# Kernel tuning notes

Hardware: AMD Instinct MI355X
Metric: run time of the kernel (lower is better)

The kernel has to match this reference:

```python
import jax, jax.numpy as jnp
import numpy as np

EMBED_DIM = 512
NUM_HEADS = 8
HEAD_DIM = EMBED_DIM // NUM_HEADS
GRID_SHAPE = (48, 48)
WINDOW = (16, 16)
BATCH = 2
SEQ = GRID_SHAPE[0] * GRID_SHAPE[1]
NEG = float(np.finfo(np.float16).min)  # matches torch.finfo(torch.float16).min fill


def build_window_mask():
    # replicates: indices = np.indices(grid).flatten(1).T; dist = |i-j|*2; all(dist < window)
    idx = np.indices(GRID_SHAPE).reshape(len(GRID_SHAPE), -1).T  # [N, 2]
    dist = np.abs(idx[:, None, :] - idx[None, :, :]) * 2          # [N, N, 2]
    mask = np.all(dist < np.array(WINDOW)[None, None, :], axis=-1)  # [N, N] bool
    return jnp.asarray(mask)


def setup_inputs() -> dict:
    key = jax.random.key(0)
    ks = jax.random.split(key, 11)
    s = 1.0 / np.sqrt(EMBED_DIM)
    inp = {
        "x_q": jax.random.normal(ks[0], (BATCH, SEQ, EMBED_DIM), jnp.float32),
        "x_k": jax.random.normal(ks[1], (BATCH, SEQ, EMBED_DIM), jnp.float32),
        "x_v": jax.random.normal(ks[2], (BATCH, SEQ, EMBED_DIM), jnp.float32),
        "Wq": jax.random.normal(ks[3], (EMBED_DIM, EMBED_DIM), jnp.float32) * s,
        "bq": jnp.zeros((EMBED_DIM,), jnp.float32),
        "Wk": jax.random.normal(ks[4], (EMBED_DIM, EMBED_DIM), jnp.float32) * s,
        "bk": jnp.zeros((EMBED_DIM,), jnp.float32),
        "Wv": jax.random.normal(ks[5], (EMBED_DIM, EMBED_DIM), jnp.float32) * s,
        "bv": jnp.zeros((EMBED_DIM,), jnp.float32),
        "Wo": jax.random.normal(ks[6], (EMBED_DIM, EMBED_DIM), jnp.float32) * s,
        "bo": jnp.zeros((EMBED_DIM,), jnp.float32),
        "attn_mask": build_window_mask(),
    }
    return inp


def reference(x_q, x_k, x_v, Wq, bq, Wk, bk, Wv, bv, Wo, bo, attn_mask):
    B, S, E = x_q.shape
    H, D = NUM_HEADS, HEAD_DIM

    def proj(x, W, b):
        y = x @ W.T + b                         # [B,S,E]
        return y.reshape(B, S, H, D).transpose(0, 2, 1, 3)  # [B,H,S,D]

    q = proj(x_q, Wq, bq)
    k = proj(x_k, Wk, bk)
    v = proj(x_v, Wv, bv)

    scores = jnp.einsum("bhqd,bhkd->bhqk", q, k) / np.sqrt(D)
    # Windowed branch: per-row gather over allowed keys + softmax == dense
    # softmax with disallowed keys masked to a huge negative value.
    scores = jnp.where(attn_mask[None, None, :, :], scores, NEG)
    probs = jax.nn.softmax(scores, axis=-1)     # dropout=0.0 -> identity
    context = jnp.einsum("bhqk,bhkd->bhqd", probs, v)
    context = context.transpose(0, 2, 1, 3).reshape(B, S, E)
    out = context @ Wo.T + bo
    return out
```

## Files before the change

### kernel.cpp

```cpp
#include <hip/hip_runtime.h>

typedef __attribute__((ext_vector_type(8))) short short8;
typedef __attribute__((ext_vector_type(4))) float f32x4;
typedef __attribute__((ext_vector_type(2))) unsigned int u32x2;

#define DEV __device__ __forceinline__

#define XQ_E 0L
#define XK_E 2359296L
#define XV_E 4718592L
#define WQ_E 7077888L
#define WK_E 7340032L
#define WV_E 7602176L
#define WO_E 7864320L
#define QH_E 8126464L
#define KH_E 10485760L
#define VT_E 12845056L
#define CTX_E 15204352L

#define LOG2E 1.4426950408889634f

#define BARRIER() __builtin_amdgcn_s_barrier()
#define SCHED0() __builtin_amdgcn_sched_barrier(0)

DEV unsigned short f2bf(float f) {
  unsigned int x = __float_as_uint(f);
  x = (x + 0x7fffu + ((x >> 16) & 1u)) >> 16;
  return (unsigned short)x;
}

DEV unsigned int pk2(float a, float b) {
  unsigned int r;
  asm("v_cvt_pk_bf16_f32 %0, %1, %2" : "=v"(r) : "v"(a), "v"(b));
  return r;
}

DEV void gl2lds16(const unsigned short* g, unsigned short* l) {
  __builtin_amdgcn_global_load_lds(
      (const __attribute__((address_space(1))) unsigned int*)g,
      (__attribute__((address_space(3))) unsigned int*)l, 16, 0, 0);
}

DEV f32x4 mfma16(short8 a, short8 b, f32x4 c) {
  return __builtin_amdgcn_mfma_f32_16x16x32_bf16(a, b, c, 0, 0, 0);
}

__global__ __launch_bounds__(256) void cvt_kernel(
    const float* __restrict__ xq, const float* __restrict__ xk,
    const float* __restrict__ xv, const float* __restrict__ wq,
    const float* __restrict__ wk, const float* __restrict__ wv,
    const float* __restrict__ wo, unsigned short* __restrict__ ws) {
  int t = blockIdx.x * 256 + threadIdx.x;
  const float* src;
  long rel, dstE;
  float sc = 1.0f;
  if (t < 1769472) {
    if (t < 589824)       { src = xq; rel = t;            dstE = XQ_E; }
    else if (t < 1179648) { src = xk; rel = t - 589824;   dstE = XK_E; }
    else                  { src = xv; rel = t - 1179648;  dstE = XV_E; }
  } else {
    int u = t - 1769472;
    if (u < 65536)        { src = wq; rel = u;            dstE = WQ_E; sc = 0.125f * LOG2E; }
    else if (u < 131072)  { src = wk; rel = u - 65536;    dstE = WK_E; }
    else if (u < 196608)  { src = wv; rel = u - 131072;   dstE = WV_E; }
    else                  { src = wo; rel = u - 196608;   dstE = WO_E; }
  }
  f32x4 v = *(const f32x4*)(src + rel * 4);
  v *= sc;
  u32x2 o;
  o.x = (unsigned int)f2bf(v.x) | ((unsigned int)f2bf(v.y) << 16);
  o.y = (unsigned int)f2bf(v.z) | ((unsigned int)f2bf(v.w) << 16);
  *(u32x2*)(ws + dstE + rel * 4) = o;
}

DEV void gemm_core(const unsigned short* __restrict__ A,
                   const unsigned short* __restrict__ W, int m0, int n0,
                   unsigned short* ldsA, unsigned short* ldsB, f32x4 acc[4][2]) {
  const int tid = threadIdx.x;
  const int lane = tid & 63, wvv = tid >> 6;
  const int g = lane >> 4, qi = lane & 15;
  const int wr = wvv >> 1, wc = wvv & 1;
#pragma unroll
  for (int mi = 0; mi < 4; ++mi)
#pragma unroll
    for (int ni = 0; ni < 2; ++ni) {
      f32x4 z = {0.f, 0.f, 0.f, 0.f};
      acc[mi][ni] = z;
    }
#define GSTAGE(bi, kt) do {                                                  \
    const int k0g = (kt) * 64;                                               \
    unsigned short* La_ = ldsA + (bi) * 8192;                                \
    unsigned short* Lb_ = ldsB + (bi) * 4096;                                \
    _Pragma("unroll")                                                        \
    for (int it = 0; it < 4; ++it) {                                         \
      int idx = it * 256 + tid;                                              \
      int row = idx >> 3, c = idx & 7, cs = c ^ (row & 7);                   \
      gl2lds16(A + (long)(m0 + row) * 512 + k0g + cs * 8, La_ + idx * 8);    \
    }                                                                        \
    _Pragma("unroll")                                                        \
    for (int it = 0; it < 2; ++it) {                                         \
      int idx = it * 256 + tid;                                              \
      int row = idx >> 3, c = idx & 7, cs = c ^ (row & 7);                   \
      gl2lds16(W + (long)(n0 + row) * 512 + k0g + cs * 8, Lb_ + idx * 8);    \
    }                                                                        \
  } while (0)
  GSTAGE(0, 0);
  GSTAGE(1, 1);
#pragma unroll
  for (int kt = 0; kt < 8; ++kt) {
    if (kt < 7) { asm volatile("s_waitcnt vmcnt(6)" ::: "memory"); }
    else        { asm volatile("s_waitcnt vmcnt(0)" ::: "memory"); }
    BARRIER();
    SCHED0();
    const unsigned short* La = ldsA + (kt & 1) * 8192;
    const unsigned short* Lb = ldsB + (kt & 1) * 4096;
    __builtin_amdgcn_s_setprio(1);
#pragma unroll
    for (int kk = 0; kk < 2; ++kk) {
      short8 af[4], bfr[2];
#pragma unroll
      for (int mi = 0; mi < 4; ++mi) {
        int row = 64 * wr + 16 * mi + qi;
        int c16 = (4 * kk + g) ^ (qi & 7);
        af[mi] = *(const short8*)(La + row * 64 + c16 * 8);
      }
#pragma unroll
      for (int ni = 0; ni < 2; ++ni) {
        int row = 32 * wc + 16 * ni + qi;
        int c16 = (4 * kk + g) ^ (qi & 7);
        bfr[ni] = *(const short8*)(Lb + row * 64 + c16 * 8);
      }
#pragma unroll
      for (int mi = 0; mi < 4; ++mi)
#pragma unroll
        for (int ni = 0; ni < 2; ++ni)
          acc[mi][ni] = mfma16(af[mi], bfr[ni], acc[mi][ni]);
    }
    __builtin_amdgcn_s_setprio(0);
    BARRIER();
    SCHED0();
    if (kt + 2 < 8) GSTAGE(kt & 1, kt + 2);
  }
#undef GSTAGE
}

__global__ __launch_bounds__(256) void proj_qkv_kernel(
    unsigned short* __restrict__ ws, const float* __restrict__ bq,
    const float* __restrict__ bk, const float* __restrict__ bv) {
  __shared__ unsigned short ldsA[2 * 8192];
  __shared__ unsigned short ldsB[2 * 4096];
  int f = blockIdx.x;
  int wid = (f & 7) * 108 + (f >> 3);
  const int z = wid / 288;
  const int rem = wid % 288;
  const int m0 = (rem >> 3) * 128, n0 = (rem & 7) * 64;
  const unsigned short *A, *W;
  const float* bias;
  unsigned short* dst;
  float bscale;
  int mode;
  if (z == 0)      { A = ws + XQ_E; W = ws + WQ_E; bias = bq; bscale = 0.125f * LOG2E; dst = ws + QH_E; mode = 0; }
  else if (z == 1) { A = ws + XK_E; W = ws + WK_E; bias = bk; bscale = 1.0f;   dst = ws + KH_E; mode = 0; }
  else             { A = ws + XV_E; W = ws + WV_E; bias = bv; bscale = 1.0f;   dst = ws + VT_E; mode = 1; }
  f32x4 acc[4][2];
  gemm_core(A, W, m0, n0, ldsA, ldsB, acc);
  const int lane = threadIdx.x & 63, wvv = threadIdx.x >> 6;
  const int g = lane >> 4, qi = lane & 15;
  const int wr = wvv >> 1, wc = wvv & 1;
#pragma unroll
  for (int ni = 0; ni < 2; ++ni) {
    int n = n0 + 32 * wc + 16 * ni + qi;
    float bb = bias[n] * bscale;
    int h = n >> 6, d = n & 63;
#pragma unroll
    for (int mi = 0; mi < 4; ++mi) {
      int m = m0 + 64 * wr + 16 * mi + 4 * g;
      int b = (m >= 2304) ? 1 : 0;
      int s = m - b * 2304;
      if (mode == 0) {
#pragma unroll
        for (int r = 0; r < 4; ++r) {
          float v = acc[mi][ni][r] + bb;
          dst[((long)((b * 8 + h) * 2304 + s + r)) * 64 + d] = f2bf(v);
        }
      } else {
        u32x2 o;
        o.x = pk2(acc[mi][ni][0] + bb, acc[mi][ni][1] + bb);
        o.y = pk2(acc[mi][ni][2] + bb, acc[mi][ni][3] + bb);
        *(u32x2*)(dst + ((long)((b * 8 + h) * 64 + d)) * 2304 + s) = o;
      }
    }
  }
}

__global__ __launch_bounds__(256) void proj_out_kernel(
    const unsigned short* __restrict__ ws, const float* __restrict__ bo,
    float* __restrict__ out) {
  __shared__ unsigned short ldsA[2 * 8192];
  __shared__ unsigned short ldsB[2 * 4096];
  int f = blockIdx.x;
  int wid = (f & 7) * 36 + (f >> 3);
  const int m0 = (wid >> 3) * 128, n0 = (wid & 7) * 64;
  f32x4 acc[4][2];
  gemm_core(ws + CTX_E, ws + WO_E, m0, n0, ldsA, ldsB, acc);
  const int lane = threadIdx.x & 63, wvv = threadIdx.x >> 6;
  const int g = lane >> 4, qi = lane & 15;
  const int wr = wvv >> 1, wc = wvv & 1;
#pragma unroll
  for (int ni = 0; ni < 2; ++ni) {
    int n = n0 + 32 * wc + 16 * ni + qi;
    float bb = bo[n];
#pragma unroll
    for (int mi = 0; mi < 4; ++mi) {
#pragma unroll
      for (int r = 0; r < 4; ++r) {
        int m = m0 + 64 * wr + 16 * mi + 4 * g + r;
        out[(long)m * 512 + n] = acc[mi][ni][r] + bb;
      }
    }
  }
}

__global__ __launch_bounds__(192) void attn_kernel(unsigned short* __restrict__ ws) {
  __shared__ unsigned short ldsKV[3 * 7168];
  __shared__ unsigned short ldsP[3][16][72];
  __shared__ unsigned short ldsDum[512];
  const int tid = threadIdx.x;
  const int lane = tid & 63, wv = tid >> 6;
  const int g = lane >> 4, qi = lane & 15;
  int f = blockIdx.x;
  int wid = (f & 7) * 96 + (f >> 3);
  const int bh = wid / 48, r = wid - 48 * bh;
  const int ci = wv * 16 + qi;
  const unsigned short* Kh = ws + KH_E + (long)bh * 2304 * 64;
  const unsigned short* Vt = ws + VT_E + (long)bh * 64 * 2304;
  const int q = r * 48 + ci;
  const unsigned short* qp = ws + QH_E + ((long)bh * 2304 + q) * 64;
  f32x4 qraw0 = *(const f32x4*)(qp + 8 * g);
  f32x4 qraw1 = *(const f32x4*)(qp + 32 + 8 * g);
  asm volatile("" : "+v"(qraw0), "+v"(qraw1));
  short8 qf0 = __builtin_bit_cast(short8, qraw0);
  short8 qf1 = __builtin_bit_cast(short8, qraw1);
  float msk[12];
#pragma unroll
  for (int mb = 0; mb < 3; ++mb)
#pragma unroll
    for (int rr = 0; rr < 4; ++rr) {
      int cj = 16 * mb + 4 * g + rr;
      msk[mb * 4 + rr] = ((unsigned)(ci - cj + 7) <= 14u) ? 0.f : -1e30f;
    }
  {
    u32x2 z2; z2.x = 0u; z2.y = 0u;
    *(u32x2*)(&ldsP[wv][qi][48 + 4 * g]) = z2;
  }
  f32x4 cacc[4];
#pragma unroll
  for (int mb = 0; mb < 4; ++mb) { f32x4 z = {0.f, 0.f, 0.f, 0.f}; cacc[mb] = z; }
  float mrun = -1e30f, lrun = 0.f;

#define ASTAGE(bi, rj) do {                                                   \
    unsigned short* Lb_ = ldsKV + (bi) * 7168;                                \
    const unsigned short* Ks_ = Kh + (long)(rj) * 3072;                       \
    _Pragma("unroll")                                                         \
    for (int it = 0; it < 5; ++it) {                                          \
      int u = it * 192 + tid;                                                 \
      if (u < 384) {                                                          \
        int kr = u >> 3, c = u & 7, cs = c ^ (kr & 7);                        \
        gl2lds16(Ks_ + kr * 64 + cs * 8, Lb_ + u * 8);                        \
      } else if (u < 896) {                                                   \
        int v2 = u - 384;                                                     \
        int d = v2 >> 3, c = v2 & 7, cs = c ^ (d & 7);                        \
        long jb = (long)(rj) * 48 + cs * 8;                                   \
        if (jb > 2296) jb = 2296;                                             \
        gl2lds16(Vt + (long)d * 2304 + jb, Lb_ + u * 8);                      \
      } else {                                                                \
        gl2lds16(Kh + (u - 896) * 8, ldsDum + (u - 896) * 8);                 \
      }                                                                       \
    }                                                                         \
  } while (0)

  const int rlo = (r > 7) ? r - 7 : 0;
  const int rhi = (r < 40) ? r + 7 : 47;
  const int nch = rhi - rlo + 1;
  ASTAGE(0, rlo);
  ASTAGE(1, rlo + 1);
  for (int t = 0; t < nch; ++t) {
    if (t + 2 < nch) ASTAGE((t + 2) % 3, rlo + t + 2);
    if (t + 3 <= nch)      { asm volatile("s_waitcnt vmcnt(10)" ::: "memory"); }
    else if (t + 2 == nch) { asm volatile("s_waitcnt vmcnt(5)" ::: "memory"); }
    else                   { asm volatile("s_waitcnt vmcnt(0)" ::: "memory"); }
    BARRIER();
    SCHED0();
    const unsigned short* Kt = ldsKV + (t % 3) * 7168;
    const unsigned short* Vm = Kt + 3072;
    f32x4 sacc[3];
#pragma unroll
    for (int mb = 0; mb < 3; ++mb) { f32x4 z = {0.f, 0.f, 0.f, 0.f}; sacc[mb] = z; }
    __builtin_amdgcn_s_setprio(1);
#pragma unroll
    for (int kk = 0; kk < 2; ++kk) {
      short8 qf = kk ? qf1 : qf0;
#pragma unroll
      for (int mb = 0; mb < 3; ++mb) {
        int row = 16 * mb + qi;
        int c16 = (4 * kk + g) ^ (qi & 7);
        short8 ka = *(const short8*)(Kt + row * 64 + c16 * 8);
        sacc[mb] = mfma16(ka, qf, sacc[mb]);
      }
    }
    __builtin_amdgcn_s_setprio(0);
    float sv[12];
    float pmax = -1e30f;
#pragma unroll
    for (int mb = 0; mb < 3; ++mb)
#pragma unroll
      for (int rr = 0; rr < 4; ++rr) {
        float s = sacc[mb][rr] + msk[mb * 4 + rr];
        sv[mb * 4 + rr] = s;
        pmax = fmaxf(pmax, s);
      }
    pmax = fmaxf(pmax, __shfl_xor(pmax, 16));
    pmax = fmaxf(pmax, __shfl_xor(pmax, 32));
    if (!__all(pmax - mrun <= 11.5f)) {
      float mnew = fmaxf(mrun, pmax);
      float scl = __builtin_amdgcn_exp2f(mrun - mnew);
      lrun *= scl;
#pragma unroll
      for (int mb = 0; mb < 4; ++mb) cacc[mb] *= scl;
      mrun = mnew;
    }
    float psum = 0.f;
    unsigned int pw[6];
#pragma unroll
    for (int mb = 0; mb < 3; ++mb) {
      float p0 = __builtin_amdgcn_exp2f(sv[mb * 4 + 0] - mrun);
      float p1 = __builtin_amdgcn_exp2f(sv[mb * 4 + 1] - mrun);
      float p2 = __builtin_amdgcn_exp2f(sv[mb * 4 + 2] - mrun);
      float p3 = __builtin_amdgcn_exp2f(sv[mb * 4 + 3] - mrun);
      psum += (p0 + p1) + (p2 + p3);
      pw[2 * mb] = pk2(p0, p1);
      pw[2 * mb + 1] = pk2(p2, p3);
    }
    psum += __shfl_xor(psum, 16);
    psum += __shfl_xor(psum, 32);
    lrun += psum;
#pragma unroll
    for (int mb = 0; mb < 3; ++mb) {
      u32x2 pv2; pv2.x = pw[2 * mb]; pv2.y = pw[2 * mb + 1];
      *(u32x2*)(&ldsP[wv][qi][16 * mb + 4 * g]) = pv2;
    }
    __builtin_amdgcn_s_setprio(1);
#pragma unroll
    for (int kk = 0; kk < 2; ++kk) {
      short8 pb = *(const short8*)(&ldsP[wv][qi][32 * kk + 8 * g]);
#pragma unroll
      for (int mb = 0; mb < 4; ++mb) {
        int row = 16 * mb + qi;
        int c16 = (4 * kk + g) ^ (qi & 7);
        short8 va = *(const short8*)(Vm + row * 64 + c16 * 8);
        cacc[mb] = mfma16(va, pb, cacc[mb]);
      }
    }
    __builtin_amdgcn_s_setprio(0);
    BARRIER();
    SCHED0();
  }
#undef ASTAGE
  const float inv = 1.0f / lrun;
  unsigned short* ctx = ws + CTX_E;
  const int b2 = bh >> 3, h2 = bh & 7;
#pragma unroll
  for (int mb = 0; mb < 4; ++mb) {
    u32x2 o;
    o.x = pk2(cacc[mb][0] * inv, cacc[mb][1] * inv);
    o.y = pk2(cacc[mb][2] * inv, cacc[mb][3] * inv);
    long off = ((long)(b2 * 2304 + q)) * 512 + h2 * 64 + 16 * mb + 4 * g;
    *(u32x2*)(ctx + off) = o;
  }
}

extern "C" void kernel_launch(void* const* d_in, const int* in_sizes, int n_in,
                              void* d_out, int out_size, void* d_ws, size_t ws_size,
                              hipStream_t stream) {
  const float* xq = (const float*)d_in[0];
  const float* xk = (const float*)d_in[1];
  const float* xv = (const float*)d_in[2];
  const float* wq = (const float*)d_in[3];
  const float* bq = (const float*)d_in[4];
  const float* wk = (const float*)d_in[5];
  const float* bk = (const float*)d_in[6];
  const float* wv = (const float*)d_in[7];
  const float* bv = (const float*)d_in[8];
  const float* wo = (const float*)d_in[9];
  const float* bo = (const float*)d_in[10];
  unsigned short* ws = (unsigned short*)d_ws;
  float* out = (float*)d_out;

  cvt_kernel<<<dim3(7936), dim3(256), 0, stream>>>(xq, xk, xv, wq, wk, wv, wo, ws);
  proj_qkv_kernel<<<dim3(864), dim3(256), 0, stream>>>(ws, bq, bk, bv);
  attn_kernel<<<dim3(768), dim3(192), 0, stream>>>(ws);
  proj_out_kernel<<<dim3(288), dim3(256), 0, stream>>>(ws, bo, out);
}
```

Before: 65.75 us.

## Fuse fp32-to-bf16 conversion into projection GEMMs via register-staged loads

Removes the separate conversion kernel and has the projection GEMMs read fp32 activations and weights directly. Tiles are loaded into registers, converted to bf16 and written to LDS, replacing async global-to-LDS copies with a register-staged double buffer. The Q scale moves from the weight to the epilogue. This drops a full pass of write-then-read traffic over the bf16 copies and one launch. In exchange each GEMM reads twice the bytes, and weights are re-converted by every block, with more register pressure and a launch bound of 3 blocks.

```diff
diff --git a/kernel.cpp b/kernel.cpp
--- a/kernel.cpp
+++ b/kernel.cpp
@@ -3,20 +3,14 @@
 typedef __attribute__((ext_vector_type(8))) short short8;
 typedef __attribute__((ext_vector_type(4))) float f32x4;
 typedef __attribute__((ext_vector_type(2))) unsigned int u32x2;
+typedef __attribute__((ext_vector_type(4))) unsigned int u32x4;
 
 #define DEV __device__ __forceinline__
 
-#define XQ_E 0L
-#define XK_E 2359296L
-#define XV_E 4718592L
-#define WQ_E 7077888L
-#define WK_E 7340032L
-#define WV_E 7602176L
-#define WO_E 7864320L
-#define QH_E 8126464L
-#define KH_E 10485760L
-#define VT_E 12845056L
-#define CTX_E 15204352L
+#define QH_E 0L
+#define KH_E 2359296L
+#define VT_E 4718592L
+#define CTX_E 7077888L
 
 #define LOG2E 1.4426950408889634f
 
@@ -45,41 +39,20 @@
   return __builtin_amdgcn_mfma_f32_16x16x32_bf16(a, b, c, 0, 0, 0);
 }
 
-__global__ __launch_bounds__(256) void cvt_kernel(
-    const float* __restrict__ xq, const float* __restrict__ xk,
-    const float* __restrict__ xv, const float* __restrict__ wq,
-    const float* __restrict__ wk, const float* __restrict__ wv,
-    const float* __restrict__ wo, unsigned short* __restrict__ ws) {
-  int t = blockIdx.x * 256 + threadIdx.x;
-  const float* src;
-  long rel, dstE;
-  float sc = 1.0f;
-  if (t < 1769472) {
-    if (t < 589824)       { src = xq; rel = t;            dstE = XQ_E; }
-    else if (t < 1179648) { src = xk; rel = t - 589824;   dstE = XK_E; }
-    else                  { src = xv; rel = t - 1179648;  dstE = XV_E; }
-  } else {
-    int u = t - 1769472;
-    if (u < 65536)        { src = wq; rel = u;            dstE = WQ_E; sc = 0.125f * LOG2E; }
-    else if (u < 131072)  { src = wk; rel = u - 65536;    dstE = WK_E; }
-    else if (u < 196608)  { src = wv; rel = u - 131072;   dstE = WV_E; }
-    else                  { src = wo; rel = u - 196608;   dstE = WO_E; }
-  }
-  f32x4 v = *(const f32x4*)(src + rel * 4);
-  v *= sc;
-  u32x2 o;
-  o.x = (unsigned int)f2bf(v.x) | ((unsigned int)f2bf(v.y) << 16);
-  o.y = (unsigned int)f2bf(v.z) | ((unsigned int)f2bf(v.w) << 16);
-  *(u32x2*)(ws + dstE + rel * 4) = o;
-}
-
-DEV void gemm_core(const unsigned short* __restrict__ A,
-                   const unsigned short* __restrict__ W, int m0, int n0,
-                   unsigned short* ldsA, unsigned short* ldsB, f32x4 acc[4][2]) {
+template <int AF32>
+DEV void gemm_rs(const float* __restrict__ Af, const unsigned short* __restrict__ Ab,
+                 const float* __restrict__ W, int m0, int n0,
+                 unsigned short* ldsA, unsigned short* ldsB, f32x4 acc[4][2]) {
   const int tid = threadIdx.x;
   const int lane = tid & 63, wvv = tid >> 6;
   const int g = lane >> 4, qi = lane & 15;
   const int wr = wvv >> 1, wc = wvv & 1;
+  const int c8 = tid & 7;
+  const int rbase = tid >> 3;
+  const int j8 = ((c8 ^ (rbase & 7))) * 8;
+  f32x4 ra[4][2];
+  u32x4 rab[4];
+  f32x4 rw[2][2];
 #pragma unroll
   for (int mi = 0; mi < 4; ++mi)
 #pragma unroll
@@ -87,31 +60,60 @@
       f32x4 z = {0.f, 0.f, 0.f, 0.f};
       acc[mi][ni] = z;
     }
-#define GSTAGE(bi, kt) do {                                                  \
-    const int k0g = (kt) * 64;                                               \
-    unsigned short* La_ = ldsA + (bi) * 8192;                                \
-    unsigned short* Lb_ = ldsB + (bi) * 4096;                                \
-    _Pragma("unroll")                                                        \
-    for (int it = 0; it < 4; ++it) {                                         \
-      int idx = it * 256 + tid;                                              \
-      int row = idx >> 3, c = idx & 7, cs = c ^ (row & 7);                   \
-      gl2lds16(A + (long)(m0 + row) * 512 + k0g + cs * 8, La_ + idx * 8);    \
-    }                                                                        \
-    _Pragma("unroll")                                                        \
-    for (int it = 0; it < 2; ++it) {                                         \
-      int idx = it * 256 + tid;                                              \
-      int row = idx >> 3, c = idx & 7, cs = c ^ (row & 7);                   \
-      gl2lds16(W + (long)(n0 + row) * 512 + k0g + cs * 8, Lb_ + idx * 8);    \
-    }                                                                        \
+#define RS_LOADS(kt) do {                                                     \
+    const int k0_ = (kt) * 64;                                                \
+    if (AF32) {                                                               \
+      _Pragma("unroll")                                                       \
+      for (int it = 0; it < 4; ++it) {                                        \
+        const float* p = Af + (long)(m0 + it * 32 + rbase) * 512 + k0_ + j8;  \
+        ra[it][0] = *(const f32x4*)p;                                         \
+        ra[it][1] = *(const f32x4*)(p + 4);                                   \
+      }                                                                       \
+    } else {                                                                  \
+      _Pragma("unroll")                                                       \
+      for (int it = 0; it < 4; ++it)                                          \
+        rab[it] = *(const u32x4*)(Ab + (long)(m0 + it * 32 + rbase) * 512 +   \
+                                  k0_ + j8);                                  \
+    }                                                                         \
+    _Pragma("unroll")                                                         \
+    for (int it = 0; it < 2; ++it) {                                          \
+      const float* p = W + (long)(n0 + it * 32 + rbase) * 512 + k0_ + j8;     \
+      rw[it][0] = *(const f32x4*)p;                                           \
+      rw[it][1] = *(const f32x4*)(p + 4);                                     \
+    }                                                                         \
   } while (0)
-  GSTAGE(0, 0);
-  GSTAGE(1, 1);
+#define RS_WRITES(bi) do {                                                    \
+    _Pragma("unroll")                                                         \
+    for (int it = 0; it < 4; ++it) {                                          \
+      u32x4 v_;                                                               \
+      if (AF32) {                                                             \
+        v_.x = pk2(ra[it][0].x, ra[it][0].y);                                 \
+        v_.y = pk2(ra[it][0].z, ra[it][0].w);                                 \
+        v_.z = pk2(ra[it][1].x, ra[it][1].y);                                 \
+        v_.w = pk2(ra[it][1].z, ra[it][1].w);                                 \
+      } else v_ = rab[it];                                                    \
+      *(u32x4*)(ldsA + (bi) * 8192 + (it * 256 + tid) * 8) = v_;              \
+    }                                                                         \
+    _Pragma("unroll")                                                         \
+    for (int it = 0; it < 2; ++it) {                                          \
+      u32x4 v_;                                                               \
+      v_.x = pk2(rw[it][0].x, rw[it][0].y);                                   \
+      v_.y = pk2(rw[it][0].z, rw[it][0].w);                                   \
+      v_.z = pk2(rw[it][1].x, rw[it][1].y);                                   \
+      v_.w = pk2(rw[it][1].z, rw[it][1].w);                                   \
+      *(u32x4*)(ldsB + (bi) * 4096 + (it * 256 + tid) * 8) = v_;              \
+    }                                                                         \
+  } while (0)
+  RS_LOADS(0);
+  RS_WRITES(0);
+  RS_LOADS(1);
+  asm volatile("s_waitcnt lgkmcnt(0)" ::: "memory");
+  BARRIER();
+  SCHED0();
 #pragma unroll
   for (int kt = 0; kt < 8; ++kt) {
-    if (kt < 7) { asm volatile("s_waitcnt vmcnt(6)" ::: "memory"); }
-    else        { asm volatile("s_waitcnt vmcnt(0)" ::: "memory"); }
-    BARRIER();
-    SCHED0();
+    if (kt < 7) RS_WRITES((kt + 1) & 1);
+    if (kt < 6) RS_LOADS(kt + 2);
     const unsigned short* La = ldsA + (kt & 1) * 8192;
     const unsigned short* Lb = ldsB + (kt & 1) * 4096;
     __builtin_amdgcn_s_setprio(1);
@@ -137,16 +139,20 @@
           acc[mi][ni] = mfma16(af[mi], bfr[ni], acc[mi][ni]);
     }
     __builtin_amdgcn_s_setprio(0);
+    asm volatile("s_waitcnt lgkmcnt(0)" ::: "memory");
     BARRIER();
     SCHED0();
-    if (kt + 2 < 8) GSTAGE(kt & 1, kt + 2);
-  }
-#undef GSTAGE
-}
-
-__global__ __launch_bounds__(256) void proj_qkv_kernel(
-    unsigned short* __restrict__ ws, const float* __restrict__ bq,
-    const float* __restrict__ bk, const float* __restrict__ bv) {
+  }
+#undef RS_LOADS
+#undef RS_WRITES
+}
+
+__global__ __launch_bounds__(256, 3) void proj_qkv_kernel(
+    const float* __restrict__ xq, const float* __restrict__ xk,
+    const float* __restrict__ xv, const float* __restrict__ wqp,
+    const float* __restrict__ wkp, const float* __restrict__ wvp,
+    const float* __restrict__ bq, const float* __restrict__ bk,
+    const float* __restrict__ bv, unsigned short* __restrict__ ws) {
   __shared__ unsigned short ldsA[2 * 8192];
   __shared__ unsigned short ldsB[2 * 4096];
   int f = blockIdx.x;
@@ -154,23 +160,22 @@
   const int z = wid / 288;
   const int rem = wid % 288;
   const int m0 = (rem >> 3) * 128, n0 = (rem & 7) * 64;
-  const unsigned short *A, *W;
-  const float* bias;
+  const float *A, *W, *bias;
   unsigned short* dst;
-  float bscale;
+  float oscale;
   int mode;
-  if (z == 0)      { A = ws + XQ_E; W = ws + WQ_E; bias = bq; bscale = 0.125f * LOG2E; dst = ws + QH_E; mode = 0; }
-  else if (z == 1) { A = ws + XK_E; W = ws + WK_E; bias = bk; bscale = 1.0f;   dst = ws + KH_E; mode = 0; }
-  else             { A = ws + XV_E; W = ws + WV_E; bias = bv; bscale = 1.0f;   dst = ws + VT_E; mode = 1; }
+  if (z == 0)      { A = xq; W = wqp; bias = bq; oscale = 0.125f * LOG2E; dst = ws + QH_E; mode = 0; }
+  else if (z == 1) { A = xk; W = wkp; bias = bk; oscale = 1.0f;           dst = ws + KH_E; mode = 0; }
+  else             { A = xv; W = wvp; bias = bv; oscale = 1.0f;           dst = ws + VT_E; mode = 1; }
   f32x4 acc[4][2];
-  gemm_core(A, W, m0, n0, ldsA, ldsB, acc);
+  gemm_rs<1>(A, nullptr, W, m0, n0, ldsA, ldsB, acc);
   const int lane = threadIdx.x & 63, wvv = threadIdx.x >> 6;
   const int g = lane >> 4, qi = lane & 15;
   const int wr = wvv >> 1, wc = wvv & 1;
 #pragma unroll
   for (int ni = 0; ni < 2; ++ni) {
     int n = n0 + 32 * wc + 16 * ni + qi;
-    float bb = bias[n] * bscale;
+    float bb = bias[n];
     int h = n >> 6, d = n & 63;
 #pragma unroll
     for (int mi = 0; mi < 4; ++mi) {
@@ -180,7 +185,7 @@
       if (mode == 0) {
 #pragma unroll
         for (int r = 0; r < 4; ++r) {
-          float v = acc[mi][ni][r] + bb;
+          float v = (acc[mi][ni][r] + bb) * oscale;
           dst[((long)((b * 8 + h) * 2304 + s + r)) * 64 + d] = f2bf(v);
         }
       } else {
@@ -193,16 +198,16 @@
   }
 }
 
-__global__ __launch_bounds__(256) void proj_out_kernel(
-    const unsigned short* __restrict__ ws, const float* __restrict__ bo,
-    float* __restrict__ out) {
+__global__ __launch_bounds__(256, 3) void proj_out_kernel(
+    const unsigned short* __restrict__ ws, const float* __restrict__ wop,
+    const float* __restrict__ bo, float* __restrict__ out) {
   __shared__ unsigned short ldsA[2 * 8192];
   __shared__ unsigned short ldsB[2 * 4096];
   int f = blockIdx.x;
   int wid = (f & 7) * 36 + (f >> 3);
   const int m0 = (wid >> 3) * 128, n0 = (wid & 7) * 64;
   f32x4 acc[4][2];
-  gemm_core(ws + CTX_E, ws + WO_E, m0, n0, ldsA, ldsB, acc);
+  gemm_rs<0>(nullptr, ws + CTX_E, wop, m0, n0, ldsA, ldsB, acc);
   const int lane = threadIdx.x & 63, wvv = threadIdx.x >> 6;
   const int g = lane >> 4, qi = lane & 15;
   const int wr = wvv >> 1, wc = wvv & 1;
@@ -396,8 +401,8 @@
   unsigned short* ws = (unsigned short*)d_ws;
   float* out = (float*)d_out;
 
-  cvt_kernel<<<dim3(7936), dim3(256), 0, stream>>>(xq, xk, xv, wq, wk, wv, wo, ws);
-  proj_qkv_kernel<<<dim3(864), dim3(256), 0, stream>>>(ws, bq, bk, bv);
+  proj_qkv_kernel<<<dim3(864), dim3(256), 0, stream>>>(xq, xk, xv, wq, wk, wv,
+                                                       bq, bk, bv, ws);
   attn_kernel<<<dim3(768), dim3(192), 0, stream>>>(ws);
-  proj_out_kernel<<<dim3(288), dim3(256), 0, stream>>>(ws, bo, out);
-}
+  proj_out_kernel<<<dim3(288), dim3(256), 0, stream>>>(ws, wo, bo, out);
+}
```

New measurement: 62.84 us. -4.4%, faster.
